# Kernel tuning notes

Hardware: AMD Instinct MI355X
Metric: run time of the kernel (lower is better)

Reference implementation:

```python
import jax, jax.numpy as jnp
import numpy as np

N = 50000
E = 800000
C = 64
NEG_SLOPE = 0.2


def gat_conv(x, edge_index, W, att_src, att_dst, bias, heads, out_ch):
    """PyG GATConv forward (concat=True, add_self_loops=True).
    x: [N, in], edge_index: [2, E] (row0=src j, row1=dst i),
    W: [in, heads*out_ch], att_src/att_dst: [heads, out_ch], bias: [heads*out_ch].
    """
    n = x.shape[0]
    loop = jnp.arange(n, dtype=edge_index.dtype)
    src = jnp.concatenate([edge_index[0], loop])
    dst = jnp.concatenate([edge_index[1], loop])

    xl = (x @ W).reshape(n, heads, out_ch)            # [N, H, F]
    a_src = jnp.einsum('nhf,hf->nh', xl, att_src)      # [N, H]
    a_dst = jnp.einsum('nhf,hf->nh', xl, att_dst)      # [N, H]

    alpha = jax.nn.leaky_relu(a_src[src] + a_dst[dst], NEG_SLOPE)  # [E', H]
    # segment softmax over incoming edges of each destination node
    amax = jax.ops.segment_max(alpha, dst, num_segments=n)
    alpha = jnp.exp(alpha - amax[dst])
    denom = jax.ops.segment_sum(alpha, dst, num_segments=n)
    alpha = alpha / denom[dst]

    # gather source features, weight, scatter-add to destinations
    msg = xl[src] * alpha[:, :, None]                  # [E', H, F]
    out = jax.ops.segment_sum(msg, dst, num_segments=n)  # [N, H, F]
    return out.reshape(n, heads * out_ch) + bias


def setup_inputs() -> dict:
    key = jax.random.key(0)
    ks = jax.random.split(key, 12)
    x = jax.random.normal(ks[0], (N, C), dtype=jnp.float32)
    undirected = jax.random.randint(ks[1], (2, E), 0, N, dtype=jnp.int32)
    directed = jax.random.randint(ks[2], (2, E), 0, N, dtype=jnp.int32)

    s1 = 1.0 / np.sqrt(C)
    s2 = 1.0 / np.sqrt(2 * C)
    W1 = jax.random.normal(ks[3], (C, 2 * C), dtype=jnp.float32) * s1
    att_src1 = jax.random.normal(ks[4], (2, C), dtype=jnp.float32) * s1
    att_dst1 = jax.random.normal(ks[5], (2, C), dtype=jnp.float32) * s1
    b1 = jnp.zeros((2 * C,), dtype=jnp.float32)

    W2 = jax.random.normal(ks[6], (2 * C, 4 * C), dtype=jnp.float32) * s2
    att_src2 = jax.random.normal(ks[7], (2, 2 * C), dtype=jnp.float32) * s2
    att_dst2 = jax.random.normal(ks[8], (2, 2 * C), dtype=jnp.float32) * s2
    b2 = jnp.zeros((4 * C,), dtype=jnp.float32)

    return {
        'x': x,
        'undirected_edges_small': undirected,
        'directed_edges_small': directed,
        'W1': W1, 'att_src1': att_src1, 'att_dst1': att_dst1, 'b1': b1,
        'W2': W2, 'att_src2': att_src2, 'att_dst2': att_dst2, 'b2': b2,
    }


def reference(x, undirected_edges_small, directed_edges_small,
              W1, att_src1, att_dst1, b1,
              W2, att_src2, att_dst2, b2):
    h = gat_conv(x, undirected_edges_small, W1, att_src1, att_dst1, b1,
                 heads=2, out_ch=C)            # [N, 2C]
    out = gat_conv(h, directed_edges_small, W2, att_src2, att_dst2, b2,
                   heads=2, out_ch=2 * C)      # [N, 4C]
    return out
```

## Files before the change

kernel.cpp:

```cpp
#include <hip/hip_runtime.h>
#include <stdint.h>

#define N_NODES 50000
#define N_EDGES 800000
#define CAP 64
#define NBUCK 400
#define BSZ 125
#define BCAP 2816
#define LOG2E 1.4426950408889634f

typedef __attribute__((ext_vector_type(8))) short bf16x8;
typedef __attribute__((ext_vector_type(4))) float f32x4;

__device__ __forceinline__ float b2f_bits(unsigned int lo16) {
    union { unsigned int i; float f; } v; v.i = lo16 << 16; return v.f;
}
__device__ __forceinline__ unsigned short f2b(float f) {
    union { float f; unsigned int i; } v; v.f = f;
    unsigned int x = v.i;
    return (unsigned short)((x + 0x7fffu + ((x >> 16) & 1u)) >> 16);
}
__device__ __forceinline__ void split2(float v, unsigned short& h, unsigned short& l) {
    h = f2b(v);
    l = f2b(v - b2f_bits(h));
}
__device__ __forceinline__ void unpack8(const uint4 u, float* f) {
    f[0] = b2f_bits(u.x & 0xffffu); f[1] = b2f_bits(u.x >> 16);
    f[2] = b2f_bits(u.y & 0xffffu); f[3] = b2f_bits(u.y >> 16);
    f[4] = b2f_bits(u.z & 0xffffu); f[5] = b2f_bits(u.z >> 16);
    f[6] = b2f_bits(u.w & 0xffffu); f[7] = b2f_bits(u.w >> 16);
}
__device__ __forceinline__ void pack8hl(const float* v, uint4& H, uint4& L) {
    unsigned short h[8], l[8];
#pragma unroll
    for (int k = 0; k < 8; ++k) split2(v[k], h[k], l[k]);
    H.x = h[0] | ((unsigned)h[1] << 16); H.y = h[2] | ((unsigned)h[3] << 16);
    H.z = h[4] | ((unsigned)h[5] << 16); H.w = h[6] | ((unsigned)h[7] << 16);
    L.x = l[0] | ((unsigned)l[1] << 16); L.y = l[2] | ((unsigned)l[3] << 16);
    L.z = l[4] | ((unsigned)l[5] << 16); L.w = l[6] | ((unsigned)l[7] << 16);
}

__global__ __launch_bounds__(256) void proj_kernel(
    const float* __restrict__ W1, const float* __restrict__ as1, const float* __restrict__ ad1,
    const float* __restrict__ b1,
    const float* __restrict__ W2, const float* __restrict__ as2, const float* __restrict__ ad2,
    float* __restrict__ P1, float* __restrict__ q2, float* __restrict__ cs,
    int* __restrict__ gcur)
{
    for (int i = threadIdx.x; i < 2 * NBUCK + 2; i += 256) gcur[i] = 0;

    __shared__ float p2[4 * 128];
    for (int i = threadIdx.x; i < 4 * 128; i += 256) {
        const int t = i >> 7, c = i & 127;
        const int h = t & 1;
        const float* att = (t < 2) ? as2 : ad2;
        float s = 0.f;
        for (int cc = 0; cc < 128; ++cc)
            s += att[h * 128 + cc] * W2[(size_t)c * 256 + h * 128 + cc];
        p2[i] = s;
    }
    {
        const int t = threadIdx.x >> 6, k = threadIdx.x & 63;
        const int h = t & 1;
        const float* att = (t < 2) ? as1 : ad1;
        float s = 0.f;
        for (int c = 0; c < 64; ++c)
            s += att[h * 64 + c] * W1[(size_t)k * 128 + h * 64 + c];
        P1[t * 64 + k] = s * LOG2E;
    }
    __syncthreads();
    for (int i = threadIdx.x; i < 4 * 128; i += 256) {
        const int t = i >> 7, j = i & 127;
        const int hc = j >> 6, k = j & 63;
        float s = 0.f;
        for (int c = 0; c < 64; ++c)
            s += W1[(size_t)k * 128 + hc * 64 + c] * p2[t * 128 + hc * 64 + c];
        q2[i] = s * LOG2E;
    }
    if (threadIdx.x < 4) {
        const int t = threadIdx.x;
        float s = 0.f;
        for (int c = 0; c < 128; ++c) s += b1[c] * p2[t * 128 + c];
        cs[t] = s * LOG2E;
    }
}

__global__ __launch_bounds__(256) void prep1_kernel(
    const float* __restrict__ X, const float* __restrict__ P1,
    const float* __restrict__ W1, const float* __restrict__ W2,
    unsigned short* __restrict__ Xh,
    float* __restrict__ a_src, float* __restrict__ a_dst,
    unsigned short* __restrict__ w1h, unsigned short* __restrict__ w1l,
    unsigned short* __restrict__ w2h, unsigned short* __restrict__ w2l,
    float* __restrict__ att2buf, int n)
{
    const int bid = blockIdx.x;
    if (bid < 128) {
        const int i = bid * 256 + threadIdx.x;
        const int nn = i >> 7, k = i & 127;
        unsigned short h, l;
        split2(W2[(size_t)k * 256 + nn], h, l);
        w2h[i] = h; w2l[i] = l;
        return;
    }
    if (bid < 160) {
        const int i = (bid - 128) * 256 + threadIdx.x;
        const int nn = i >> 6, k = i & 63;
        unsigned short h, l;
        split2(W1[(size_t)k * 128 + nn], h, l);
        w1h[i] = h; w1l[i] = l;
        return;
    }
    const int gid = (bid - 160) * 256 + threadIdx.x;
    if (gid < n) ((float4*)att2buf)[gid] = make_float4(0.f, 0.f, 0.f, 0.f);
    const int node = gid >> 4;
    const int sl = threadIdx.x & 15;
    if (node >= n) return;
    const float4 v = *(const float4*)(X + (size_t)node * 64 + sl * 4);
    ushort4 hv;
    hv.x = f2b(v.x); hv.y = f2b(v.y); hv.z = f2b(v.z); hv.w = f2b(v.w);
    *(ushort4*)(Xh + (size_t)node * 64 + sl * 4) = hv;
    float d[4];
#pragma unroll
    for (int t = 0; t < 4; ++t) {
        const float* pp = P1 + t * 64 + sl * 4;
        d[t] = v.x * pp[0] + v.y * pp[1] + v.z * pp[2] + v.w * pp[3];
    }
#pragma unroll
    for (int o = 1; o < 16; o <<= 1)
#pragma unroll
        for (int t = 0; t < 4; ++t) d[t] += __shfl_xor(d[t], o);
    if (sl == 0) {
        *(float2*)(a_src + node * 2) = make_float2(d[0], d[1]);
        *(float2*)(a_dst + node * 2) = make_float2(d[2], d[3]);
    }
}

__global__ __launch_bounds__(256) void bucket_kernel(
    const int* __restrict__ e1, const int* __restrict__ e2, int ne,
    int* __restrict__ gcur, unsigned int* __restrict__ stage)
{
    const int layer = blockIdx.x & 1;
    const int bslot = blockIdx.x >> 1;
    const int nbl = gridDim.x >> 1;
    const int* __restrict__ eix = layer ? e2 : e1;
    int* cur = gcur + layer * NBUCK;
    unsigned int* __restrict__ stg = stage + (size_t)layer * NBUCK * BCAP;

    __shared__ int cnt_lds[NBUCK];
    __shared__ int base_lds[NBUCK];
    constexpr int EPT = 16;
    constexpr int CHUNK = 256 * EPT;

    for (int base = bslot * CHUNK; base < ne; base += nbl * CHUNK) {
        for (int i = threadIdx.x; i < NBUCK; i += 256) cnt_lds[i] = 0;
        __syncthreads();

        unsigned int rec[EPT];
        int bk[EPT];
#pragma unroll
        for (int i = 0; i < EPT; ++i) {
            const int e = base + i * 256 + threadIdx.x;
            bk[i] = -1;
            if (e < ne) {
                const int s = eix[e];
                const int d = eix[ne + e];
                if ((unsigned)d < (unsigned)N_NODES) {
                    const int b = d / BSZ;
                    bk[i] = b;
                    rec[i] = (unsigned)s | ((unsigned)(d - b * BSZ) << 16);
                    atomicAdd(&cnt_lds[b], 1);
                }
            }
        }
        __syncthreads();
        for (int i = threadIdx.x; i < NBUCK; i += 256) {
            const int c = cnt_lds[i];
            base_lds[i] = c ? atomicAdd(&cur[i], c) : 0;
            cnt_lds[i] = 0;
        }
        __syncthreads();
#pragma unroll
        for (int i = 0; i < EPT; ++i) {
            if (bk[i] >= 0) {
                const int idx = base_lds[bk[i]] + atomicAdd(&cnt_lds[bk[i]], 1);
                if (idx < BCAP) stg[(size_t)bk[i] * BCAP + idx] = rec[i];
            }
        }
        __syncthreads();
    }
}

__global__ __launch_bounds__(256) void place_kernel(
    const unsigned int* __restrict__ stage, const int* __restrict__ gcur,
    int* __restrict__ gtot,
    unsigned int* __restrict__ offs1, unsigned int* __restrict__ offs2,
    unsigned short* __restrict__ ss1, unsigned short* __restrict__ ss2)
{
    const int layer = blockIdx.x & 1;
    const int bucket = blockIdx.x >> 1;
    int m = gcur[layer * NBUCK + bucket];
    m = m < BCAP ? m : BCAP;
    const unsigned int* __restrict__ stg =
        stage + ((size_t)(layer * NBUCK + bucket)) * BCAP;
    unsigned int* __restrict__ offs = layer ? offs2 : offs1;
    unsigned short* __restrict__ ss = layer ? ss2 : ss1;
    const int d0 = bucket * BSZ;

    __shared__ int c_lds[BSZ];
    __shared__ int pref[BSZ + 1];
    __shared__ int baseSh;
    __shared__ unsigned short img[BCAP];

    for (int i = threadIdx.x; i < BSZ; i += 256) c_lds[i] = 0;
    __syncthreads();

    for (int i = threadIdx.x; i < m; i += 256)
        atomicAdd(&c_lds[stg[i] >> 16], 1);
    __syncthreads();

    if (threadIdx.x == 0) {
        int run = 0;
        for (int i = 0; i < BSZ; ++i) {
            int c = c_lds[i]; c = c < CAP ? c : CAP;
            pref[i] = run; run += c;
        }
        pref[BSZ] = run;
        baseSh = atomicAdd(&gtot[layer], run);
    }
    __syncthreads();
    const int base = baseSh;
    for (int i = threadIdx.x; i < BSZ; i += 256) {
        int c = c_lds[i]; c = c < CAP ? c : CAP;
        offs[d0 + i] = ((unsigned)(base + pref[i]) << 7) | (unsigned)c;
        c_lds[i] = 0;
    }
    __syncthreads();

    for (int i = threadIdx.x; i < m; i += 256) {
        const unsigned int v = stg[i];
        const int dr = (int)(v >> 16);
        const int slot = atomicAdd(&c_lds[dr], 1);
        if (slot < CAP) img[pref[dr] + slot] = (unsigned short)(v & 0xffffu);
    }
    __syncthreads();

    unsigned short* out = ss + base;
    const int tot = pref[BSZ];
    for (int i = threadIdx.x; i < tot; i += 256) out[i] = img[i];
}

__global__ __launch_bounds__(256) void agg1_kernel(
    const unsigned short* __restrict__ XH, const float* __restrict__ X,
    const float* __restrict__ a_src, const float* __restrict__ a_dst,
    const unsigned int* __restrict__ offs, const unsigned short* __restrict__ bins,
    unsigned short* __restrict__ AH, unsigned short* __restrict__ AL, int n)
{
    const int node = (blockIdx.x * 256 + threadIdx.x) >> 6;
    const int lane = threadIdx.x & 63;
    if (node >= n) return;
    const int hl = lane & 7;
    const int sub = lane >> 3;

    const unsigned o = offs[node];
    const int start = (int)(o >> 7);
    const int deg = (int)(o & 127);
    const int e = start + deg;
    const float2 ad = *(const float2*)(a_dst + node * 2);

    float2 As; float4 sva, svb;
    if (sub == 0) {
        As = *(const float2*)(a_src + node * 2);
        sva = *(const float4*)(X + (size_t)node * 64 + hl * 8);
        svb = *(const float4*)(X + (size_t)node * 64 + hl * 8 + 4);
    }

    float acc0[8] = {0.f,0.f,0.f,0.f,0.f,0.f,0.f,0.f};
    float acc1[8] = {0.f,0.f,0.f,0.f,0.f,0.f,0.f,0.f};
    float den0 = 0.f, den1 = 0.f;

    int p = start;
    int jc = 0; float2 Ac = make_float2(0.f, 0.f); uint4 uc = make_uint4(0,0,0,0);
    if (p < e) {
        const int pos = p + sub;
        const int pc = pos < e ? pos : e - 1;
        jc = bins[pc];
        Ac = *(const float2*)(a_src + jc * 2);
        uc = *(const uint4*)(XH + (size_t)jc * 64 + hl * 8);
    }
    while (p < e) {
        const int pn = p + 8;
        int jn = 0; float2 An; uint4 un;
        const bool more = pn < e;
        if (more) {
            const int pos = pn + sub;
            const int pc = pos < e ? pos : e - 1;
            jn = bins[pc];
            An = *(const float2*)(a_src + jn * 2);
            un = *(const uint4*)(XH + (size_t)jn * 64 + hl * 8);
        }
        float l0 = Ac.x + ad.x; l0 = fmaxf(l0, 0.2f * l0);
        float l1 = Ac.y + ad.y; l1 = fmaxf(l1, 0.2f * l1);
        float w0 = __builtin_amdgcn_exp2f(l0);
        float w1 = __builtin_amdgcn_exp2f(l1);
        if (p + sub >= e) { w0 = 0.f; w1 = 0.f; }
        den0 += w0; den1 += w1;
        float f[8]; unpack8(uc, f);
#pragma unroll
        for (int k = 0; k < 8; ++k) { acc0[k] += w0 * f[k]; acc1[k] += w1 * f[k]; }
        if (!more) break;
        jc = jn; Ac = An; uc = un; p = pn;
    }
    if (sub == 0) {
        float l0 = As.x + ad.x; l0 = fmaxf(l0, 0.2f * l0);
        float l1 = As.y + ad.y; l1 = fmaxf(l1, 0.2f * l1);
        const float w0 = __builtin_amdgcn_exp2f(l0);
        const float w1 = __builtin_amdgcn_exp2f(l1);
        den0 += w0; den1 += w1;
        float f[8] = {sva.x, sva.y, sva.z, sva.w, svb.x, svb.y, svb.z, svb.w};
#pragma unroll
        for (int k = 0; k < 8; ++k) { acc0[k] += w0 * f[k]; acc1[k] += w1 * f[k]; }
    }
#pragma unroll
    for (int o2 = 8; o2 < 64; o2 <<= 1) {
        den0 += __shfl_xor(den0, o2); den1 += __shfl_xor(den1, o2);
#pragma unroll
        for (int k = 0; k < 8; ++k) {
            acc0[k] += __shfl_xor(acc0[k], o2);
            acc1[k] += __shfl_xor(acc1[k], o2);
        }
    }
    if (sub < 2) {
        const int head = sub;
        const float inv = 1.f / (head ? den1 : den0);
        float vv[8];
#pragma unroll
        for (int k = 0; k < 8; ++k) vv[k] = (head ? acc1[k] : acc0[k]) * inv;
        uint4 H, L;
        pack8hl(vv, H, L);
        const size_t off = (size_t)head * N_NODES * 64 + (size_t)node * 64 + hl * 8;
        *(uint4*)(AH + off) = H;
        *(uint4*)(AL + off) = L;
    }
}

__global__ __launch_bounds__(256) void agg2_kernel(
    const unsigned short* __restrict__ HH, const unsigned short* __restrict__ HL,
    const float* __restrict__ a_src, const float* __restrict__ a_dst,
    const float* __restrict__ cs,
    const unsigned int* __restrict__ offs, const unsigned short* __restrict__ bins,
    unsigned short* __restrict__ AH, unsigned short* __restrict__ AL, int n)
{
    const int node = (blockIdx.x * 256 + threadIdx.x) >> 6;
    const int lane = threadIdx.x & 63;
    if (node >= n) return;
    const int hl = lane & 15;
    const int sub = lane >> 4;

    const float4 csv = *(const float4*)cs;
    const float C0 = csv.x + csv.z, C1 = csv.y + csv.w;

    const unsigned o = offs[node];
    const int start = (int)(o >> 7);
    const int deg = (int)(o & 127);
    const int e = start + deg;
    const float2 ad = *(const float2*)(a_dst + node * 2);
    const float ad0 = ad.x + C0, ad1 = ad.y + C1;

    float2 As; uint4 suh, sul;
    if (sub == 0) {
        As = *(const float2*)(a_src + node * 2);
        suh = *(const uint4*)(HH + (size_t)node * 128 + hl * 8);
        sul = *(const uint4*)(HL + (size_t)node * 128 + hl * 8);
    }

    float acc0[8] = {0.f,0.f,0.f,0.f,0.f,0.f,0.f,0.f};
    float acc1[8] = {0.f,0.f,0.f,0.f,0.f,0.f,0.f,0.f};
    float den0 = 0.f, den1 = 0.f;

    int p = start;
    int jc = 0; float2 Ac = make_float2(0.f, 0.f); uint4 uc = make_uint4(0,0,0,0);
    if (p < e) {
        const int pos = p + sub;
        const int pc = pos < e ? pos : e - 1;
        jc = bins[pc];
        Ac = *(const float2*)(a_src + jc * 2);
        uc = *(const uint4*)(HH + (size_t)jc * 128 + hl * 8);
    }
    while (p < e) {
        const int pn = p + 4;
        int jn = 0; float2 An; uint4 un;
        const bool more = pn < e;
        if (more) {
            const int pos = pn + sub;
            const int pc = pos < e ? pos : e - 1;
            jn = bins[pc];
            An = *(const float2*)(a_src + jn * 2);
            un = *(const uint4*)(HH + (size_t)jn * 128 + hl * 8);
        }
        float l0 = Ac.x + ad0; l0 = fmaxf(l0, 0.2f * l0);
        float l1 = Ac.y + ad1; l1 = fmaxf(l1, 0.2f * l1);
        float w0 = __builtin_amdgcn_exp2f(l0);
        float w1 = __builtin_amdgcn_exp2f(l1);
        if (p + sub >= e) { w0 = 0.f; w1 = 0.f; }
        den0 += w0; den1 += w1;
        float f[8]; unpack8(uc, f);
#pragma unroll
        for (int k = 0; k < 8; ++k) { acc0[k] += w0 * f[k]; acc1[k] += w1 * f[k]; }
        if (!more) break;
        jc = jn; Ac = An; uc = un; p = pn;
    }
    if (sub == 0) {
        float l0 = As.x + ad0; l0 = fmaxf(l0, 0.2f * l0);
        float l1 = As.y + ad1; l1 = fmaxf(l1, 0.2f * l1);
        const float w0 = __builtin_amdgcn_exp2f(l0);
        const float w1 = __builtin_amdgcn_exp2f(l1);
        den0 += w0; den1 += w1;
        float fh[8], fl[8];
        unpack8(suh, fh); unpack8(sul, fl);
#pragma unroll
        for (int k = 0; k < 8; ++k) {
            const float f = fh[k] + fl[k];
            acc0[k] += w0 * f; acc1[k] += w1 * f;
        }
    }
#pragma unroll
    for (int o2 = 16; o2 < 64; o2 <<= 1) {
        den0 += __shfl_xor(den0, o2); den1 += __shfl_xor(den1, o2);
#pragma unroll
        for (int k = 0; k < 8; ++k) {
            acc0[k] += __shfl_xor(acc0[k], o2);
            acc1[k] += __shfl_xor(acc1[k], o2);
        }
    }
    if (sub < 2) {
        const int head = sub;
        const float inv = 1.f / (head ? den1 : den0);
        float vv[8];
#pragma unroll
        for (int k = 0; k < 8; ++k) vv[k] = (head ? acc1[k] : acc0[k]) * inv;
        uint4 H, L;
        pack8hl(vv, H, L);
        const size_t off = (size_t)head * N_NODES * 128 + (size_t)node * 128 + hl * 8;
        *(uint4*)(AH + off) = H;
        *(uint4*)(AL + off) = L;
    }
}

__global__ __launch_bounds__(512) void gemm_h_kernel(
    const unsigned short* __restrict__ AH, const unsigned short* __restrict__ AL,
    const unsigned short* __restrict__ WTh, const unsigned short* __restrict__ WTl,
    const float* __restrict__ b1, const float* __restrict__ q2,
    unsigned short* __restrict__ HH, unsigned short* __restrict__ HL,
    float* __restrict__ a_src2, float* __restrict__ a_dst2, int M)
{
    constexpr int K = 64, KC = 2;
    const int wave = threadIdx.x >> 6;
    const int lane = threadIdx.x & 63;
    const int head = wave >> 2;
    const int c0 = (wave & 3) * 16;
    const int lr = lane & 15;
    const int lk = (lane >> 4) * 8;
    const int colg = head * 64 + c0 + ((lane >> 4) << 2);
    const bool doAtt = (wave & 3) == 0;

    bf16x8 awh[KC], awl[KC];
    {
        const unsigned short* wr  = WTh + (size_t)(head * 64 + c0 + lr) * K + lk;
        const unsigned short* wr2 = WTl + (size_t)(head * 64 + c0 + lr) * K + lk;
#pragma unroll
        for (int c = 0; c < KC; ++c) {
            awh[c] = *(const bf16x8*)(wr + c * 32);
            awl[c] = *(const bf16x8*)(wr2 + c * 32);
        }
    }
    const float4 bias = *(const float4*)(b1 + colg);
    const unsigned short* XhB = AH + (size_t)head * M * 64;
    const unsigned short* XlB = AL + (size_t)head * M * 64;

    auto loadB = [&](bf16x8 (&bh)[KC], bf16x8 (&bl)[KC], int sidx) {
        const unsigned short* xr  = XhB + (size_t)(sidx * 16 + lr) * 64 + lk;
        const unsigned short* xr2 = XlB + (size_t)(sidx * 16 + lr) * 64 + lk;
#pragma unroll
        for (int c = 0; c < KC; ++c) {
            bh[c] = *(const bf16x8*)(xr + c * 32);
            bl[c] = *(const bf16x8*)(xr2 + c * 32);
        }
    };
    auto compute = [&](bf16x8 (&bh)[KC], bf16x8 (&bl)[KC], int sidx) {
        f32x4 acc = {0.f, 0.f, 0.f, 0.f};
#pragma unroll
        for (int c = 0; c < KC; ++c)
            acc = __builtin_amdgcn_mfma_f32_16x16x32_bf16(awh[c], bh[c], acc, 0, 0, 0);
#pragma unroll
        for (int c = 0; c < KC; ++c)
            acc = __builtin_amdgcn_mfma_f32_16x16x32_bf16(awh[c], bl[c], acc, 0, 0, 0);
#pragma unroll
        for (int c = 0; c < KC; ++c)
            acc = __builtin_amdgcn_mfma_f32_16x16x32_bf16(awl[c], bh[c], acc, 0, 0, 0);
        ushort4 hv, lv;
        split2(acc[0] + bias.x, hv.x, lv.x); split2(acc[1] + bias.y, hv.y, lv.y);
        split2(acc[2] + bias.z, hv.z, lv.z); split2(acc[3] + bias.w, hv.w, lv.w);
        const size_t o = (size_t)(sidx * 16 + lr) * 128 + colg;
        *(ushort4*)(HH + o) = hv;
        *(ushort4*)(HL + o) = lv;
        if (doAtt) {
            float P[4] = {0.f, 0.f, 0.f, 0.f};
#pragma unroll
            for (int c = 0; c < KC; ++c)
#pragma unroll
                for (int i = 0; i < 8; ++i) {
                    const float v = b2f_bits((unsigned short)bh[c][i])
                                  + b2f_bits((unsigned short)bl[c][i]);
                    const int kk = head * 64 + lk + c * 32 + i;
#pragma unroll
                    for (int t = 0; t < 4; ++t) P[t] += v * q2[t * 128 + kk];
                }
#pragma unroll
            for (int o2 = 16; o2 < 64; o2 <<= 1)
#pragma unroll
                for (int t = 0; t < 4; ++t) P[t] += __shfl_xor(P[t], o2);
            if (lane < 16) {
                const int m = sidx * 16 + lane;
                atomicAdd(&a_src2[m * 2 + 0], P[0]);
                atomicAdd(&a_src2[m * 2 + 1], P[1]);
                atomicAdd(&a_dst2[m * 2 + 0], P[2]);
                atomicAdd(&a_dst2[m * 2 + 1], P[3]);
            }
        }
    };

    const int NSTRIP = M / 16;
    const int nb = gridDim.x;
    int s = blockIdx.x;
    bf16x8 b0h[KC], b0l[KC], b1h_[KC], b1l_[KC];
    if (s < NSTRIP) loadB(b0h, b0l, s);
    while (s < NSTRIP) {
        const int sn = s + nb;
        if (sn < NSTRIP) loadB(b1h_, b1l_, sn);
        compute(b0h, b0l, s);
        if (sn >= NSTRIP) break;
        const int sn2 = sn + nb;
        if (sn2 < NSTRIP) loadB(b0h, b0l, sn2);
        compute(b1h_, b1l_, sn);
        s = sn2;
    }
}

__global__ __launch_bounds__(512) void gemm_out_kernel(
    const unsigned short* __restrict__ AH, const unsigned short* __restrict__ AL,
    const unsigned short* __restrict__ WTh, const unsigned short* __restrict__ WTl,
    const float* __restrict__ b2,
    float* __restrict__ OUT, int M)
{
    constexpr int K = 128, KC = 4, CT = 2;
    const int wave = threadIdx.x >> 6;
    const int lane = threadIdx.x & 63;
    const int head = wave >> 2;
    const int c0 = (wave & 3) * 32;
    const int lr = lane & 15;
    const int lk = (lane >> 4) * 8;

    bf16x8 awh[CT][KC], awl[CT][KC];
    float4 bias[CT];
    int colg[CT];
#pragma unroll
    for (int t = 0; t < CT; ++t) {
        const unsigned short* wr  = WTh + (size_t)(head * 128 + c0 + t * 16 + lr) * K + lk;
        const unsigned short* wr2 = WTl + (size_t)(head * 128 + c0 + t * 16 + lr) * K + lk;
#pragma unroll
        for (int c = 0; c < KC; ++c) {
            awh[t][c] = *(const bf16x8*)(wr + c * 32);
            awl[t][c] = *(const bf16x8*)(wr2 + c * 32);
        }
        colg[t] = head * 128 + c0 + t * 16 + ((lane >> 4) << 2);
        bias[t] = *(const float4*)(b2 + colg[t]);
    }
    const unsigned short* XhB = AH + (size_t)head * M * 128;
    const unsigned short* XlB = AL + (size_t)head * M * 128;

    auto loadB = [&](bf16x8 (&bh)[KC], bf16x8 (&bl)[KC], int sidx) {
        const unsigned short* xr  = XhB + (size_t)(sidx * 16 + lr) * 128 + lk;
        const unsigned short* xr2 = XlB + (size_t)(sidx * 16 + lr) * 128 + lk;
#pragma unroll
        for (int c = 0; c < KC; ++c) {
            bh[c] = *(const bf16x8*)(xr + c * 32);
            bl[c] = *(const bf16x8*)(xr2 + c * 32);
        }
    };
    auto compute = [&](bf16x8 (&bh)[KC], bf16x8 (&bl)[KC], int sidx) {
#pragma unroll
        for (int t = 0; t < CT; ++t) {
            f32x4 acc = {0.f, 0.f, 0.f, 0.f};
#pragma unroll
            for (int c = 0; c < KC; ++c)
                acc = __builtin_amdgcn_mfma_f32_16x16x32_bf16(awh[t][c], bh[c], acc, 0, 0, 0);
#pragma unroll
            for (int c = 0; c < KC; ++c)
                acc = __builtin_amdgcn_mfma_f32_16x16x32_bf16(awh[t][c], bl[c], acc, 0, 0, 0);
#pragma unroll
            for (int c = 0; c < KC; ++c)
                acc = __builtin_amdgcn_mfma_f32_16x16x32_bf16(awl[t][c], bh[c], acc, 0, 0, 0);
            float4 o;
            o.x = acc[0] + bias[t].x; o.y = acc[1] + bias[t].y;
            o.z = acc[2] + bias[t].z; o.w = acc[3] + bias[t].w;
            *(float4*)(OUT + (size_t)(sidx * 16 + lr) * 256 + colg[t]) = o;
        }
    };

    const int NSTRIP = M / 16;
    const int nb = gridDim.x;
    int s = blockIdx.x;
    bf16x8 b0h[KC], b0l[KC], b1h_[KC], b1l_[KC];
    if (s < NSTRIP) loadB(b0h, b0l, s);
    while (s < NSTRIP) {
        const int sn = s + nb;
        if (sn < NSTRIP) loadB(b1h_, b1l_, sn);
        compute(b0h, b0l, s);
        if (sn >= NSTRIP) break;
        const int sn2 = sn + nb;
        if (sn2 < NSTRIP) loadB(b0h, b0l, sn2);
        compute(b1h_, b1l_, sn);
        s = sn2;
    }
}

extern "C" void kernel_launch(void* const* d_in, const int* in_sizes, int n_in,
                              void* d_out, int out_size, void* d_ws, size_t ws_size,
                              hipStream_t stream)
{
    const int N = N_NODES, E = N_EDGES;

    const float* x   = (const float*)d_in[0];
    const int*   und = (const int*)d_in[1];
    const int*   dir = (const int*)d_in[2];
    const float* W1  = (const float*)d_in[3];
    const float* as1 = (const float*)d_in[4];
    const float* ad1 = (const float*)d_in[5];
    const float* b1  = (const float*)d_in[6];
    const float* W2  = (const float*)d_in[7];
    const float* as2 = (const float*)d_in[8];
    const float* ad2 = (const float*)d_in[9];
    const float* b2  = (const float*)d_in[10];

    char* p = (char*)d_ws;
    auto alloc = [&](size_t bytes) {
        char* r = p;
        p += (bytes + 255) & ~(size_t)255;
        return r;
    };
    unsigned short* agg2h = (unsigned short*)alloc((size_t)2 * N * 128 * 2);
    unsigned short* agg2l = (unsigned short*)alloc((size_t)2 * N * 128 * 2);
    unsigned short* hhbuf = (unsigned short*)alloc((size_t)N * 128 * 2);
    unsigned short* hlbuf = (unsigned short*)alloc((size_t)N * 128 * 2);
    unsigned short* ss1   = (unsigned short*)alloc((size_t)E * 2);
    unsigned short* ss2   = (unsigned short*)alloc((size_t)E * 2);
    unsigned int* offs1 = (unsigned int*)alloc((size_t)N * 4);
    unsigned int* offs2 = (unsigned int*)alloc((size_t)N * 4);
    float* a_src1 = (float*)alloc((size_t)N * 2 * 4);
    float* a_dst1 = (float*)alloc((size_t)N * 2 * 4);
    float* att2buf = (float*)alloc((size_t)N * 4 * 4);
    int*   gcur  = (int*)alloc(((size_t)2 * NBUCK + 2) * 4);
    unsigned short* w1th = (unsigned short*)alloc((size_t)128 * 64 * 2);
    unsigned short* w1tl = (unsigned short*)alloc((size_t)128 * 64 * 2);
    unsigned short* w2th = (unsigned short*)alloc((size_t)256 * 128 * 2);
    unsigned short* w2tl = (unsigned short*)alloc((size_t)256 * 128 * 2);
    float* P1d = (float*)alloc(4 * 64 * 4);
    float* q2d = (float*)alloc(4 * 128 * 4);
    float* csd = (float*)alloc(4 * 4);
    int* gtot = gcur + 2 * NBUCK;
    float* a_src2 = att2buf, * a_dst2 = att2buf + (size_t)N * 2;

    unsigned int* stage = (unsigned int*)agg2h;
    unsigned short* x1h   = (unsigned short*)d_out;
    unsigned short* agg1h = (unsigned short*)d_out + (size_t)N * 64;
    unsigned short* agg1l = (unsigned short*)d_out + (size_t)N * 64 + (size_t)N * 128;

    const int WB = (N * 64) / 256;

    proj_kernel<<<1, 256, 0, stream>>>(W1, as1, ad1, b1, W2, as2, ad2,
                                       P1d, q2d, csd, gcur);
    bucket_kernel<<<2 * 196, 256, 0, stream>>>(und, dir, E, gcur, stage);
    place_kernel<<<2 * NBUCK, 256, 0, stream>>>(stage, gcur, gtot,
                                                offs1, offs2, ss1, ss2);
    prep1_kernel<<<160 + (N * 16) / 256, 256, 0, stream>>>(
        x, P1d, W1, W2, x1h, a_src1, a_dst1,
        w1th, w1tl, w2th, w2tl, att2buf, N);

    agg1_kernel<<<WB, 256, 0, stream>>>(x1h, x, a_src1, a_dst1, offs1, ss1,
                                        agg1h, agg1l, N);
    gemm_h_kernel<<<768, 512, 0, stream>>>(agg1h, agg1l, w1th, w1tl, b1, q2d,
                                           hhbuf, hlbuf, a_src2, a_dst2, N);

    agg2_kernel<<<WB, 256, 0, stream>>>(hhbuf, hlbuf, a_src2, a_dst2, csd,
                                        offs2, ss2, agg2h, agg2l, N);
    gemm_out_kernel<<<512, 512, 0, stream>>>(agg2h, agg2l, w2th, w2tl, b2,
                                             (float*)d_out, N);
}
```

Before: 295.8 us.

## Map one node per lane subgroup with degree-sorted node order in aggregation

The aggregation kernels now give each 8-lane (layer 1) or 16-lane (layer 2) subgroup its own destination node, instead of splitting one node's edges across a whole wave. This removes the cross-subgroup shuffle reductions and the masked tail iterations. To keep subgroups in a wave busy for similar times, place_kernel now builds a per-bucket ordering of nodes sorted by degree, and the aggregation kernels read nodes through it. The trade-off is a plain serial edge loop with no software prefetch, an extra order array, and some extra LDS work in place_kernel.

```diff
diff --git a/kernel.cpp b/kernel.cpp
--- a/kernel.cpp
+++ b/kernel.cpp
@@ -195,7 +195,8 @@
     const unsigned int* __restrict__ stage, const int* __restrict__ gcur,
     int* __restrict__ gtot,
     unsigned int* __restrict__ offs1, unsigned int* __restrict__ offs2,
-    unsigned short* __restrict__ ss1, unsigned short* __restrict__ ss2)
+    unsigned short* __restrict__ ss1, unsigned short* __restrict__ ss2,
+    unsigned short* __restrict__ order1, unsigned short* __restrict__ order2)
 {
     const int layer = blockIdx.x & 1;
     const int bucket = blockIdx.x >> 1;
@@ -205,12 +206,14 @@
         stage + ((size_t)(layer * NBUCK + bucket)) * BCAP;
     unsigned int* __restrict__ offs = layer ? offs2 : offs1;
     unsigned short* __restrict__ ss = layer ? ss2 : ss1;
+    unsigned short* __restrict__ order = layer ? order2 : order1;
     const int d0 = bucket * BSZ;
 
     __shared__ int c_lds[BSZ];
     __shared__ int pref[BSZ + 1];
     __shared__ int baseSh;
     __shared__ unsigned short img[BCAP];
+    __shared__ int dh[CAP + 1];
 
     for (int i = threadIdx.x; i < BSZ; i += 256) c_lds[i] = 0;
     __syncthreads();
@@ -235,6 +238,7 @@
         offs[d0 + i] = ((unsigned)(base + pref[i]) << 7) | (unsigned)c;
         c_lds[i] = 0;
     }
+    for (int i = threadIdx.x; i <= CAP; i += 256) dh[i] = 0;
     __syncthreads();
 
     for (int i = threadIdx.x; i < m; i += 256) {
@@ -248,100 +252,82 @@
     unsigned short* out = ss + base;
     const int tot = pref[BSZ];
     for (int i = threadIdx.x; i < tot; i += 256) out[i] = img[i];
+
+    for (int i = threadIdx.x; i < BSZ; i += 256)
+        atomicAdd(&dh[pref[i + 1] - pref[i]], 1);
+    __syncthreads();
+    if (threadIdx.x == 0) {
+        int run = 0;
+        for (int i = 0; i <= CAP; ++i) { const int c = dh[i]; dh[i] = run; run += c; }
+    }
+    __syncthreads();
+    for (int i = threadIdx.x; i < BSZ; i += 256) {
+        const int r = atomicAdd(&dh[pref[i + 1] - pref[i]], 1);
+        order[d0 + r] = (unsigned short)(d0 + i);
+    }
 }
 
 __global__ __launch_bounds__(256) void agg1_kernel(
     const unsigned short* __restrict__ XH, const float* __restrict__ X,
     const float* __restrict__ a_src, const float* __restrict__ a_dst,
     const unsigned int* __restrict__ offs, const unsigned short* __restrict__ bins,
+    const unsigned short* __restrict__ order,
     unsigned short* __restrict__ AH, unsigned short* __restrict__ AL, int n)
 {
-    const int node = (blockIdx.x * 256 + threadIdx.x) >> 6;
+    const int wid = (blockIdx.x * 256 + threadIdx.x) >> 6;
     const int lane = threadIdx.x & 63;
-    if (node >= n) return;
     const int hl = lane & 7;
     const int sub = lane >> 3;
+    const int base = wid * 8;
+    if (base >= n) return;
+    const int node = order[base + sub];
 
     const unsigned o = offs[node];
     const int start = (int)(o >> 7);
     const int deg = (int)(o & 127);
-    const int e = start + deg;
     const float2 ad = *(const float2*)(a_dst + node * 2);
 
-    float2 As; float4 sva, svb;
-    if (sub == 0) {
-        As = *(const float2*)(a_src + node * 2);
-        sva = *(const float4*)(X + (size_t)node * 64 + hl * 8);
-        svb = *(const float4*)(X + (size_t)node * 64 + hl * 8 + 4);
-    }
-
-    float acc0[8] = {0.f,0.f,0.f,0.f,0.f,0.f,0.f,0.f};
-    float acc1[8] = {0.f,0.f,0.f,0.f,0.f,0.f,0.f,0.f};
+    float acc0[8] = {0,0,0,0,0,0,0,0}, acc1[8] = {0,0,0,0,0,0,0,0};
     float den0 = 0.f, den1 = 0.f;
 
-    int p = start;
-    int jc = 0; float2 Ac = make_float2(0.f, 0.f); uint4 uc = make_uint4(0,0,0,0);
-    if (p < e) {
-        const int pos = p + sub;
-        const int pc = pos < e ? pos : e - 1;
-        jc = bins[pc];
-        Ac = *(const float2*)(a_src + jc * 2);
-        uc = *(const uint4*)(XH + (size_t)jc * 64 + hl * 8);
-    }
-    while (p < e) {
-        const int pn = p + 8;
-        int jn = 0; float2 An; uint4 un;
-        const bool more = pn < e;
-        if (more) {
-            const int pos = pn + sub;
-            const int pc = pos < e ? pos : e - 1;
-            jn = bins[pc];
-            An = *(const float2*)(a_src + jn * 2);
-            un = *(const uint4*)(XH + (size_t)jn * 64 + hl * 8);
-        }
-        float l0 = Ac.x + ad.x; l0 = fmaxf(l0, 0.2f * l0);
-        float l1 = Ac.y + ad.y; l1 = fmaxf(l1, 0.2f * l1);
-        float w0 = __builtin_amdgcn_exp2f(l0);
-        float w1 = __builtin_amdgcn_exp2f(l1);
-        if (p + sub >= e) { w0 = 0.f; w1 = 0.f; }
-        den0 += w0; den1 += w1;
-        float f[8]; unpack8(uc, f);
-#pragma unroll
-        for (int k = 0; k < 8; ++k) { acc0[k] += w0 * f[k]; acc1[k] += w1 * f[k]; }
-        if (!more) break;
-        jc = jn; Ac = An; uc = un; p = pn;
-    }
-    if (sub == 0) {
-        float l0 = As.x + ad.x; l0 = fmaxf(l0, 0.2f * l0);
-        float l1 = As.y + ad.y; l1 = fmaxf(l1, 0.2f * l1);
+    for (int i = 0; i < deg; ++i) {
+        const int j = bins[start + i];
+        const float2 A = *(const float2*)(a_src + j * 2);
+        const uint4 u = *(const uint4*)(XH + (size_t)j * 64 + hl * 8);
+        float l0 = A.x + ad.x; l0 = fmaxf(l0, 0.2f * l0);
+        float l1 = A.y + ad.y; l1 = fmaxf(l1, 0.2f * l1);
         const float w0 = __builtin_amdgcn_exp2f(l0);
         const float w1 = __builtin_amdgcn_exp2f(l1);
         den0 += w0; den1 += w1;
-        float f[8] = {sva.x, sva.y, sva.z, sva.w, svb.x, svb.y, svb.z, svb.w};
+        float f[8]; unpack8(u, f);
 #pragma unroll
         for (int k = 0; k < 8; ++k) { acc0[k] += w0 * f[k]; acc1[k] += w1 * f[k]; }
     }
-#pragma unroll
-    for (int o2 = 8; o2 < 64; o2 <<= 1) {
-        den0 += __shfl_xor(den0, o2); den1 += __shfl_xor(den1, o2);
-#pragma unroll
-        for (int k = 0; k < 8; ++k) {
-            acc0[k] += __shfl_xor(acc0[k], o2);
-            acc1[k] += __shfl_xor(acc1[k], o2);
-        }
-    }
-    if (sub < 2) {
-        const int head = sub;
-        const float inv = 1.f / (head ? den1 : den0);
-        float vv[8];
-#pragma unroll
-        for (int k = 0; k < 8; ++k) vv[k] = (head ? acc1[k] : acc0[k]) * inv;
-        uint4 H, L;
-        pack8hl(vv, H, L);
-        const size_t off = (size_t)head * N_NODES * 64 + (size_t)node * 64 + hl * 8;
-        *(uint4*)(AH + off) = H;
-        *(uint4*)(AL + off) = L;
-    }
+    {
+        const float2 A = *(const float2*)(a_src + node * 2);
+        const float4 va = *(const float4*)(X + (size_t)node * 64 + hl * 8);
+        const float4 vb = *(const float4*)(X + (size_t)node * 64 + hl * 8 + 4);
+        float l0 = A.x + ad.x; l0 = fmaxf(l0, 0.2f * l0);
+        float l1 = A.y + ad.y; l1 = fmaxf(l1, 0.2f * l1);
+        const float w0 = __builtin_amdgcn_exp2f(l0);
+        const float w1 = __builtin_amdgcn_exp2f(l1);
+        den0 += w0; den1 += w1;
+        float f[8] = {va.x, va.y, va.z, va.w, vb.x, vb.y, vb.z, vb.w};
+#pragma unroll
+        for (int k = 0; k < 8; ++k) { acc0[k] += w0 * f[k]; acc1[k] += w1 * f[k]; }
+    }
+    const float inv0 = 1.f / den0, inv1 = 1.f / den1;
+    float v0[8], v1[8];
+#pragma unroll
+    for (int k = 0; k < 8; ++k) { v0[k] = acc0[k] * inv0; v1[k] = acc1[k] * inv1; }
+    uint4 H0, L0, H1, L1;
+    pack8hl(v0, H0, L0);
+    pack8hl(v1, H1, L1);
+    const size_t o0 = (size_t)node * 64 + hl * 8;
+    *(uint4*)(AH + o0) = H0;
+    *(uint4*)(AL + o0) = L0;
+    *(uint4*)(AH + (size_t)N_NODES * 64 + o0) = H1;
+    *(uint4*)(AL + (size_t)N_NODES * 64 + o0) = L1;
 }
 
 __global__ __launch_bounds__(256) void agg2_kernel(
@@ -349,13 +335,16 @@
     const float* __restrict__ a_src, const float* __restrict__ a_dst,
     const float* __restrict__ cs,
     const unsigned int* __restrict__ offs, const unsigned short* __restrict__ bins,
+    const unsigned short* __restrict__ order,
     unsigned short* __restrict__ AH, unsigned short* __restrict__ AL, int n)
 {
-    const int node = (blockIdx.x * 256 + threadIdx.x) >> 6;
+    const int wid = (blockIdx.x * 256 + threadIdx.x) >> 6;
     const int lane = threadIdx.x & 63;
-    if (node >= n) return;
     const int hl = lane & 15;
     const int sub = lane >> 4;
+    const int base = wid * 4;
+    if (base >= n) return;
+    const int node = order[base + sub];
 
     const float4 csv = *(const float4*)cs;
     const float C0 = csv.x + csv.z, C1 = csv.y + csv.w;
@@ -363,88 +352,54 @@
     const unsigned o = offs[node];
     const int start = (int)(o >> 7);
     const int deg = (int)(o & 127);
-    const int e = start + deg;
     const float2 ad = *(const float2*)(a_dst + node * 2);
     const float ad0 = ad.x + C0, ad1 = ad.y + C1;
 
-    float2 As; uint4 suh, sul;
-    if (sub == 0) {
-        As = *(const float2*)(a_src + node * 2);
-        suh = *(const uint4*)(HH + (size_t)node * 128 + hl * 8);
-        sul = *(const uint4*)(HL + (size_t)node * 128 + hl * 8);
-    }
-
-    float acc0[8] = {0.f,0.f,0.f,0.f,0.f,0.f,0.f,0.f};
-    float acc1[8] = {0.f,0.f,0.f,0.f,0.f,0.f,0.f,0.f};
+    float acc0[8] = {0,0,0,0,0,0,0,0}, acc1[8] = {0,0,0,0,0,0,0,0};
     float den0 = 0.f, den1 = 0.f;
 
-    int p = start;
-    int jc = 0; float2 Ac = make_float2(0.f, 0.f); uint4 uc = make_uint4(0,0,0,0);
-    if (p < e) {
-        const int pos = p + sub;
-        const int pc = pos < e ? pos : e - 1;
-        jc = bins[pc];
-        Ac = *(const float2*)(a_src + jc * 2);
-        uc = *(const uint4*)(HH + (size_t)jc * 128 + hl * 8);
-    }
-    while (p < e) {
-        const int pn = p + 4;
-        int jn = 0; float2 An; uint4 un;
-        const bool more = pn < e;
-        if (more) {
-            const int pos = pn + sub;
-            const int pc = pos < e ? pos : e - 1;
-            jn = bins[pc];
-            An = *(const float2*)(a_src + jn * 2);
-            un = *(const uint4*)(HH + (size_t)jn * 128 + hl * 8);
-        }
-        float l0 = Ac.x + ad0; l0 = fmaxf(l0, 0.2f * l0);
-        float l1 = Ac.y + ad1; l1 = fmaxf(l1, 0.2f * l1);
-        float w0 = __builtin_amdgcn_exp2f(l0);
-        float w1 = __builtin_amdgcn_exp2f(l1);
-        if (p + sub >= e) { w0 = 0.f; w1 = 0.f; }
+    for (int i = 0; i < deg; ++i) {
+        const int j = bins[start + i];
+        const float2 A = *(const float2*)(a_src + j * 2);
+        const uint4 u = *(const uint4*)(HH + (size_t)j * 128 + hl * 8);
+        float l0 = A.x + ad0; l0 = fmaxf(l0, 0.2f * l0);
+        float l1 = A.y + ad1; l1 = fmaxf(l1, 0.2f * l1);
+        const float w0 = __builtin_amdgcn_exp2f(l0);
+        const float w1 = __builtin_amdgcn_exp2f(l1);
         den0 += w0; den1 += w1;
-        float f[8]; unpack8(uc, f);
+        float f[8]; unpack8(u, f);
 #pragma unroll
         for (int k = 0; k < 8; ++k) { acc0[k] += w0 * f[k]; acc1[k] += w1 * f[k]; }
-        if (!more) break;
-        jc = jn; Ac = An; uc = un; p = pn;
-    }
-    if (sub == 0) {
-        float l0 = As.x + ad0; l0 = fmaxf(l0, 0.2f * l0);
-        float l1 = As.y + ad1; l1 = fmaxf(l1, 0.2f * l1);
+    }
+    {
+        const float2 A = *(const float2*)(a_src + node * 2);
+        const uint4 uh = *(const uint4*)(HH + (size_t)node * 128 + hl * 8);
+        const uint4 ul = *(const uint4*)(HL + (size_t)node * 128 + hl * 8);
+        float l0 = A.x + ad0; l0 = fmaxf(l0, 0.2f * l0);
+        float l1 = A.y + ad1; l1 = fmaxf(l1, 0.2f * l1);
         const float w0 = __builtin_amdgcn_exp2f(l0);
         const float w1 = __builtin_amdgcn_exp2f(l1);
         den0 += w0; den1 += w1;
         float fh[8], fl[8];
-        unpack8(suh, fh); unpack8(sul, fl);
+        unpack8(uh, fh); unpack8(ul, fl);
 #pragma unroll
         for (int k = 0; k < 8; ++k) {
             const float f = fh[k] + fl[k];
             acc0[k] += w0 * f; acc1[k] += w1 * f;
         }
     }
-#pragma unroll
-    for (int o2 = 16; o2 < 64; o2 <<= 1) {
-        den0 += __shfl_xor(den0, o2); den1 += __shfl_xor(den1, o2);
-#pragma unroll
-        for (int k = 0; k < 8; ++k) {
-            acc0[k] += __shfl_xor(acc0[k], o2);
-            acc1[k] += __shfl_xor(acc1[k], o2);
-        }
-    }
-    if (sub < 2) {
-        const int head = sub;
-        const float inv = 1.f / (head ? den1 : den0);
-        float vv[8];
-#pragma unroll
-        for (int k = 0; k < 8; ++k) vv[k] = (head ? acc1[k] : acc0[k]) * inv;
-        uint4 H, L;
-        pack8hl(vv, H, L);
-        const size_t off = (size_t)head * N_NODES * 128 + (size_t)node * 128 + hl * 8;
-        *(uint4*)(AH + off) = H;
-        *(uint4*)(AL + off) = L;
-    }
+    const float inv0 = 1.f / den0, inv1 = 1.f / den1;
+    float v0[8], v1[8];
+#pragma unroll
+    for (int k = 0; k < 8; ++k) { v0[k] = acc0[k] * inv0; v1[k] = acc1[k] * inv1; }
+    uint4 H0, L0, H1, L1;
+    pack8hl(v0, H0, L0);
+    pack8hl(v1, H1, L1);
+    const size_t o0 = (size_t)node * 128 + hl * 8;
+    *(uint4*)(AH + o0) = H0;
+    *(uint4*)(AL + o0) = L0;
+    *(uint4*)(AH + (size_t)N_NODES * 128 + o0) = H1;
+    *(uint4*)(AL + (size_t)N_NODES * 128 + o0) = L1;
 }
 
 __global__ __launch_bounds__(512) void gemm_h_kernel(
@@ -657,6 +612,8 @@
     unsigned short* ss2   = (unsigned short*)alloc((size_t)E * 2);
     unsigned int* offs1 = (unsigned int*)alloc((size_t)N * 4);
     unsigned int* offs2 = (unsigned int*)alloc((size_t)N * 4);
+    unsigned short* order1 = (unsigned short*)alloc((size_t)N * 2);
+    unsigned short* order2 = (unsigned short*)alloc((size_t)N * 2);
     float* a_src1 = (float*)alloc((size_t)N * 2 * 4);
     float* a_dst1 = (float*)alloc((size_t)N * 2 * 4);
     float* att2buf = (float*)alloc((size_t)N * 4 * 4);
@@ -674,26 +631,25 @@
     unsigned int* stage = (unsigned int*)agg2h;
     unsigned short* x1h   = (unsigned short*)d_out;
     unsigned short* agg1h = (unsigned short*)d_out + (size_t)N * 64;
-    unsigned short* agg1l = (unsigned short*)d_out + (size_t)N * 64 + (size_t)N * 128;
-
-    const int WB = (N * 64) / 256;
+    unsigned short* agg1l = (unsigned short*)d_out + (size_t)N * 64 + (size_t)2 * N * 64;
 
     proj_kernel<<<1, 256, 0, stream>>>(W1, as1, ad1, b1, W2, as2, ad2,
                                        P1d, q2d, csd, gcur);
     bucket_kernel<<<2 * 196, 256, 0, stream>>>(und, dir, E, gcur, stage);
     place_kernel<<<2 * NBUCK, 256, 0, stream>>>(stage, gcur, gtot,
-                                                offs1, offs2, ss1, ss2);
+                                                offs1, offs2, ss1, ss2,
+                                                order1, order2);
     prep1_kernel<<<160 + (N * 16) / 256, 256, 0, stream>>>(
         x, P1d, W1, W2, x1h, a_src1, a_dst1,
         w1th, w1tl, w2th, w2tl, att2buf, N);
 
-    agg1_kernel<<<WB, 256, 0, stream>>>(x1h, x, a_src1, a_dst1, offs1, ss1,
-                                        agg1h, agg1l, N);
+    agg1_kernel<<<(N / 8 + 3) / 4, 256, 0, stream>>>(
+        x1h, x, a_src1, a_dst1, offs1, ss1, order1, agg1h, agg1l, N);
     gemm_h_kernel<<<768, 512, 0, stream>>>(agg1h, agg1l, w1th, w1tl, b1, q2d,
                                            hhbuf, hlbuf, a_src2, a_dst2, N);
 
-    agg2_kernel<<<WB, 256, 0, stream>>>(hhbuf, hlbuf, a_src2, a_dst2, csd,
-                                        offs2, ss2, agg2h, agg2l, N);
+    agg2_kernel<<<N / 16, 256, 0, stream>>>(
+        hhbuf, hlbuf, a_src2, a_dst2, csd, offs2, ss2, order2, agg2h, agg2l, N);
     gemm_out_kernel<<<512, 512, 0, stream>>>(agg2h, agg2l, w2th, w2tl, b2,
                                              (float*)d_out, N);
 }
```

New measurement: 287.4 us. -2.9%, faster.
